# Performance work log

Hardware: AMD Instinct MI355X
Metric: run time of the kernel (lower is better)

The kernel has to match this reference:

```python
import jax, jax.numpy as jnp
import numpy as np

N = 100000   # nodes
E = 1600000  # edges
IN = 128     # in_dim
H = 64       # hidden_dim
EPS = 1e-5


def layer_norm(x, g, b):
    mu = x.mean(-1, keepdims=True)
    v = ((x - mu) ** 2).mean(-1, keepdims=True)
    return (x - mu) * jax.lax.rsqrt(v + EPS) * g + b


def gcn_conv(x, W, b, src, dst, dinv):
    # PyG GCNConv: x' = D^{-1/2}(A+I)D^{-1/2} X W + b (degrees include self-loops)
    h = x @ W                                   # [N, H]
    coef = dinv[src] * dinv[dst]                # [E]
    agg = jax.ops.segment_sum(h[src] * coef[:, None], dst, num_segments=N)
    agg = agg + h * (dinv * dinv)[:, None]      # self-loop term
    return agg + b


def setup_inputs() -> dict:
    key = jax.random.key(0)
    ks = jax.random.split(key, 12)
    inp = {
        "x": jax.random.normal(ks[0], (N, IN), jnp.float32),
        "edge_index": jax.random.randint(ks[1], (2, E), 0, N, dtype=jnp.int64
                                         if jax.config.jax_enable_x64 else jnp.int32),
    }
    dims = [(IN, H), (H, H), (H, H)]
    for i, (di, do) in enumerate(dims, start=1):
        inp[f"W{i}"] = jax.random.normal(ks[2 * i], (di, do), jnp.float32) / np.sqrt(di)
        inp[f"b{i}"] = jnp.zeros((do,), jnp.float32)
        inp[f"g{i}"] = jnp.ones((do,), jnp.float32)
        inp[f"be{i}"] = jnp.zeros((do,), jnp.float32)
    inp["Wh"] = jax.random.normal(ks[11], (H, 1), jnp.float32) / np.sqrt(H)
    inp["bh"] = jnp.zeros((1,), jnp.float32)
    return inp


def reference(x, edge_index, W1, b1, g1, be1, W2, b2, g2, be2, W3, b3, g3, be3, Wh, bh):
    src, dst = edge_index[0], edge_index[1]
    deg = jax.ops.segment_sum(jnp.ones((E,), x.dtype), dst, num_segments=N) + 1.0
    dinv = jax.lax.rsqrt(deg)
    for W, b, g, be in ((W1, b1, g1, be1), (W2, b2, g2, be2), (W3, b3, g3, be3)):
        x = gcn_conv(x, W, b, src, dst, dinv)
        x = layer_norm(x, g, be)
        x = jax.nn.gelu(x, approximate=False)  # F.gelu default = exact erf
        # dropout omitted (eval mode / deterministic reference)
    return (x @ Wh + bh).squeeze(-1)  # [N]
```

## Files before the change

### kernel.cpp

```cpp
#include <hip/hip_runtime.h>
#include <math.h>

#define NODES 100000
#define EDGES 1600000
#define SCAN_CHUNK 1024
#define NBUCK 196
#define BCAP2 12288
#define EPB 4096

typedef __attribute__((ext_vector_type(8))) short short8;
typedef __attribute__((ext_vector_type(4))) float floatx4;
typedef __attribute__((ext_vector_type(4))) unsigned uv4;

__device__ __forceinline__ float gsum8(float x) {
#pragma unroll
  for (int o = 4; o > 0; o >>= 1) x += __shfl_xor(x, o, 64);
  return x;
}

__device__ __forceinline__ short f2bf(float f) {
  union { float f; unsigned u; } v;
  v.f = f;
  unsigned r = 0x7fffu + ((v.u >> 16) & 1u);
  return (short)((v.u + r) >> 16);
}
__device__ __forceinline__ float bflo(unsigned p) {
  union { unsigned u; float f; } v; v.u = p << 16; return v.f;
}
__device__ __forceinline__ float bfhi(unsigned p) {
  union { unsigned u; float f; } v; v.u = p & 0xffff0000u; return v.f;
}

__global__ __launch_bounds__(256) void k_bin2(const int* __restrict__ src,
                                              const int* __restrict__ dst,
                                              int* __restrict__ bins,
                                              int* __restrict__ gcur) {
  __shared__ int cnt[NBUCK], gbase[NBUCK], lcur[NBUCK];
  int t = threadIdx.x;
  for (int i = t; i < NBUCK; i += 256) cnt[i] = 0;
  __syncthreads();
  int base = blockIdx.x * EPB;
  int s[16], d[16];
#pragma unroll
  for (int j = 0; j < 16; ++j) {
    int e = base + j * 256 + t;
    if (e < EDGES) {
      s[j] = src[e];
      d[j] = dst[e];
      atomicAdd(&cnt[d[j] >> 9], 1);
    } else {
      d[j] = -1;
    }
  }
  __syncthreads();
  for (int i = t; i < NBUCK; i += 256) {
    int c = cnt[i];
    gbase[i] = c ? atomicAdd(&gcur[i], c) : 0;
    lcur[i] = 0;
  }
  __syncthreads();
#pragma unroll
  for (int j = 0; j < 16; ++j) {
    if (d[j] >= 0) {
      int bk = d[j] >> 9;
      int lp = atomicAdd(&lcur[bk], 1);
      int pos = gbase[bk] + lp;
      if (pos < BCAP2) bins[bk * BCAP2 + pos] = s[j] | ((d[j] & 511) << 17);
    }
  }
}

__global__ __launch_bounds__(256) void k_hist(const int* __restrict__ bins,
                                              const int* __restrict__ gcur,
                                              int* __restrict__ deg,
                                              float* __restrict__ dinv) {
  __shared__ int cnt[512];
  int b = blockIdx.x, t = threadIdx.x;
  cnt[t] = 0; cnt[t + 256] = 0;
  __syncthreads();
  int c = gcur[b]; if (c > BCAP2) c = BCAP2;
  const int* bp = &bins[b * BCAP2];
  for (int i = t; i < c; i += 256)
    atomicAdd(&cnt[(bp[i] >> 17) & 511], 1);
  __syncthreads();
#pragma unroll
  for (int k = 0; k < 2; ++k) {
    int n = b * 512 + t + k * 256;
    if (n < NODES) {
      int cc = cnt[t + k * 256];
      deg[n] = cc;
      dinv[n] = rsqrtf((float)cc + 1.0f);
    }
  }
}

__global__ void k_scan1(const int* __restrict__ deg, int* __restrict__ part) {
  __shared__ int sw[4];
  int b = blockIdx.x, t = threadIdx.x;
  int base = b * SCAN_CHUNK;
  int s = 0;
#pragma unroll
  for (int j = 0; j < 4; ++j) {
    int i = base + t * 4 + j;
    if (i < NODES) s += deg[i];
  }
  for (int o = 32; o > 0; o >>= 1) s += __shfl_xor(s, o, 64);
  if ((t & 63) == 0) sw[t >> 6] = s;
  __syncthreads();
  if (t == 0) part[b] = sw[0] + sw[1] + sw[2] + sw[3];
}

__global__ void k_scan2(int* part, int nb) {
  __shared__ int sm[128];
  int t = threadIdx.x;
  int v = (t < nb) ? part[t] : 0;
  sm[t] = v;
  __syncthreads();
  for (int o = 1; o < 128; o <<= 1) {
    int u = (t >= o) ? sm[t - o] : 0;
    __syncthreads();
    sm[t] += u;
    __syncthreads();
  }
  if (t < nb) part[t] = sm[t] - v;
}

__global__ void k_scan3(const int* __restrict__ deg, const int* __restrict__ part,
                        int* __restrict__ rowptr) {
  __shared__ int wtot[4];
  int b = blockIdx.x, t = threadIdx.x;
  int lane = t & 63, wid = t >> 6;
  int base = b * SCAN_CHUNK;
  int d[4];
  int s = 0;
#pragma unroll
  for (int j = 0; j < 4; ++j) {
    int i = base + t * 4 + j;
    d[j] = (i < NODES) ? deg[i] : 0;
    s += d[j];
  }
  int inc = s;
#pragma unroll
  for (int o = 1; o < 64; o <<= 1) {
    int u = __shfl_up(inc, o, 64);
    if (lane >= o) inc += u;
  }
  if (lane == 63) wtot[wid] = inc;
  __syncthreads();
  int wpre = 0;
  for (int w = 0; w < wid; ++w) wpre += wtot[w];
  int off = part[b] + wpre + inc - s;
#pragma unroll
  for (int j = 0; j < 4; ++j) {
    int i = base + t * 4 + j;
    if (i < NODES) { rowptr[i] = off; off += d[j]; }
  }
  if (b == 0 && t == 0) rowptr[NODES] = EDGES;
}

__global__ __launch_bounds__(256) void k_fillb(const int* __restrict__ bins,
                                               const int* __restrict__ gcur,
                                               const int* __restrict__ rowptr,
                                               int* __restrict__ csr) {
  __shared__ int cur[512];
  int b = blockIdx.x, t = threadIdx.x;
#pragma unroll
  for (int k = 0; k < 2; ++k) {
    int n = b * 512 + t + k * 256;
    cur[t + k * 256] = (n < NODES) ? rowptr[n] : 0;
  }
  __syncthreads();
  int c = gcur[b]; if (c > BCAP2) c = BCAP2;
  const int* bp = &bins[b * BCAP2];
  for (int i = t; i < c; i += 256) {
    int pk = bp[i];
    int p = atomicAdd(&cur[(pk >> 17) & 511], 1);
    csr[p] = pk & 0x1FFFF;
  }
}

template <int K>
__global__ __launch_bounds__(256) void k_gemm_f32(const float* __restrict__ x,
                                                  const float* __restrict__ W,
                                                  const float* __restrict__ dinv,
                                                  short* __restrict__ hs) {
  constexpr int KP = K + 8;
  __shared__ short wt[64 * KP];
  for (int idx = threadIdx.x; idx < K * 64; idx += 256) {
    int k = idx >> 6, n = idx & 63;
    wt[n * KP + k] = f2bf(W[idx]);
  }
  __syncthreads();
  int wid = threadIdx.x >> 6, lane = threadIdx.x & 63;
  int tile = blockIdx.x * 4 + wid;
  if (tile * 16 >= NODES) return;
  int m = lane & 15, q = lane >> 4;

  short8 bfr[4][K / 32];
#pragma unroll
  for (int ct = 0; ct < 4; ++ct)
#pragma unroll
    for (int ks = 0; ks < K / 32; ++ks)
      bfr[ct][ks] = *reinterpret_cast<const short8*>(&wt[(ct * 16 + m) * KP + ks * 32 + q * 8]);

  floatx4 acc[4];
#pragma unroll
  for (int ct = 0; ct < 4; ++ct) acc[ct] = {0.f, 0.f, 0.f, 0.f};
  int r0 = tile * 16;
#pragma unroll
  for (int ks = 0; ks < K / 32; ++ks) {
    const float* xp = &x[(size_t)(r0 + m) * K + ks * 32 + q * 8];
    floatx4 a0 = *reinterpret_cast<const floatx4*>(xp);
    floatx4 a1 = *reinterpret_cast<const floatx4*>(xp + 4);
    short8 af;
#pragma unroll
    for (int j = 0; j < 4; ++j) { af[j] = f2bf(a0[j]); af[4 + j] = f2bf(a1[j]); }
#pragma unroll
    for (int ct = 0; ct < 4; ++ct)
      acc[ct] = __builtin_amdgcn_mfma_f32_16x16x32_bf16(af, bfr[ct][ks], acc[ct], 0, 0, 0);
  }
  float dv[4];
#pragma unroll
  for (int r = 0; r < 4; ++r) dv[r] = dinv[r0 + q * 4 + r];
#pragma unroll
  for (int ct = 0; ct < 4; ++ct)
#pragma unroll
    for (int r = 0; r < 4; ++r) {
      int row = r0 + q * 4 + r, col = ct * 16 + m;
      hs[row * 64 + col] = f2bf(acc[ct][r] * dv[r]);
    }
}

__global__ __launch_bounds__(256) void k_gemm_bf(const short* __restrict__ x,
                                                 const float* __restrict__ W,
                                                 const float* __restrict__ dinv,
                                                 short* __restrict__ hs) {
  constexpr int K = 64, KP = K + 8;
  __shared__ short wt[64 * KP];
  for (int idx = threadIdx.x; idx < K * 64; idx += 256) {
    int k = idx >> 6, n = idx & 63;
    wt[n * KP + k] = f2bf(W[idx]);
  }
  __syncthreads();
  int wid = threadIdx.x >> 6, lane = threadIdx.x & 63;
  int tile = blockIdx.x * 4 + wid;
  if (tile * 16 >= NODES) return;
  int m = lane & 15, q = lane >> 4;

  short8 bfr[4][2];
#pragma unroll
  for (int ct = 0; ct < 4; ++ct)
#pragma unroll
    for (int ks = 0; ks < 2; ++ks)
      bfr[ct][ks] = *reinterpret_cast<const short8*>(&wt[(ct * 16 + m) * KP + ks * 32 + q * 8]);

  floatx4 acc[4];
#pragma unroll
  for (int ct = 0; ct < 4; ++ct) acc[ct] = {0.f, 0.f, 0.f, 0.f};
  int r0 = tile * 16;
#pragma unroll
  for (int ks = 0; ks < 2; ++ks) {
    short8 af = *reinterpret_cast<const short8*>(&x[(size_t)(r0 + m) * K + ks * 32 + q * 8]);
#pragma unroll
    for (int ct = 0; ct < 4; ++ct)
      acc[ct] = __builtin_amdgcn_mfma_f32_16x16x32_bf16(af, bfr[ct][ks], acc[ct], 0, 0, 0);
  }
  float dv[4];
#pragma unroll
  for (int r = 0; r < 4; ++r) dv[r] = dinv[r0 + q * 4 + r];
#pragma unroll
  for (int ct = 0; ct < 4; ++ct)
#pragma unroll
    for (int r = 0; r < 4; ++r) {
      int row = r0 + q * 4 + r, col = ct * 16 + m;
      hs[row * 64 + col] = f2bf(acc[ct][r] * dv[r]);
    }
}

template <int FINAL>
__global__ __launch_bounds__(256) void k_agg(const short* __restrict__ hs,
                                             const float* __restrict__ dinv,
                                             const int* __restrict__ rowptr,
                                             const int* __restrict__ csr,
                                             const float* __restrict__ bias,
                                             const float* __restrict__ gam,
                                             const float* __restrict__ bet,
                                             const float* __restrict__ Wh,
                                             const float* __restrict__ bh,
                                             void* __restrict__ out) {
  const uv4* hsv = (const uv4*)hs;
  int lane = threadIdx.x & 63, wid = threadIdx.x >> 6;
  int g = lane >> 3, q = lane & 7;
  int n = blockIdx.x * 32 + wid * 8 + g;
  int e0 = rowptr[n], e1 = rowptr[n + 1];
  float dn = dinv[n];
  uv4 sv = hsv[(size_t)n * 8 + q];
  float acc[8];
#pragma unroll
  for (int w = 0; w < 4; ++w) { acc[2 * w] = bflo(sv[w]); acc[2 * w + 1] = bfhi(sv[w]); }

  int srcb = lane & 0x38;
  for (int base = e0; base < e1; base += 8) {
    int cnt = e1 - base;
    if (cnt > 8) cnt = 8;
    int a = base + (q < cnt ? q : 0);
    int sidx = csr[a];
    int s[8];
#pragma unroll
    for (int j = 0; j < 8; ++j) s[j] = __shfl(sidx, srcb | j, 64);
    uv4 v[8];
#pragma unroll
    for (int j = 0; j < 8; ++j) v[j] = hsv[(size_t)s[j] * 8 + q];
    if (cnt == 8) {
#pragma unroll
      for (int j = 0; j < 8; ++j)
#pragma unroll
        for (int w = 0; w < 4; ++w) { acc[2 * w] += bflo(v[j][w]); acc[2 * w + 1] += bfhi(v[j][w]); }
    } else {
#pragma unroll
      for (int j = 0; j < 8; ++j)
        if (j < cnt)
#pragma unroll
          for (int w = 0; w < 4; ++w) { acc[2 * w] += bflo(v[j][w]); acc[2 * w + 1] += bfhi(v[j][w]); }
    }
  }

  const floatx4* bi4 = (const floatx4*)bias;
  floatx4 b0 = bi4[q * 2], b1 = bi4[q * 2 + 1];
#pragma unroll
  for (int f = 0; f < 4; ++f) { acc[f] = acc[f] * dn + b0[f]; acc[f + 4] = acc[f + 4] * dn + b1[f]; }

  float lsum = 0.f;
#pragma unroll
  for (int f = 0; f < 8; ++f) lsum += acc[f];
  float mu = gsum8(lsum) * (1.0f / 64.0f);
  float d[8], lvar = 0.f;
#pragma unroll
  for (int f = 0; f < 8; ++f) { d[f] = acc[f] - mu; lvar += d[f] * d[f]; }
  float rs = rsqrtf(gsum8(lvar) * (1.0f / 64.0f) + 1e-5f);
  const floatx4* gm4 = (const floatx4*)gam;
  const floatx4* bt4 = (const floatx4*)bet;
  floatx4 g0 = gm4[q * 2], g1 = gm4[q * 2 + 1];
  floatx4 t0 = bt4[q * 2], t1 = bt4[q * 2 + 1];
  float u[8];
#pragma unroll
  for (int f = 0; f < 8; ++f) {
    float gv = (f < 4) ? g0[f] : g1[f - 4];
    float tv = (f < 4) ? t0[f] : t1[f - 4];
    float vv = d[f] * rs * gv + tv;
    u[f] = 0.5f * vv * (1.0f + erff(vv * 0.70710678118654752f));
  }
  if (FINAL) {
    const floatx4* wh4 = (const floatx4*)Wh;
    floatx4 w0 = wh4[q * 2], w1 = wh4[q * 2 + 1];
    float lp = 0.f;
#pragma unroll
    for (int f = 0; f < 4; ++f) lp += u[f] * w0[f] + u[f + 4] * w1[f];
    float p = gsum8(lp);
    if (q == 0) ((float*)out)[n] = p + bh[0];
  } else {
    uv4 pk;
#pragma unroll
    for (int w = 0; w < 4; ++w)
      pk[w] = (unsigned)(unsigned short)f2bf(u[2 * w]) |
              ((unsigned)(unsigned short)f2bf(u[2 * w + 1]) << 16);
    ((uv4*)out)[(size_t)n * 8 + q] = pk;
  }
}

extern "C" void kernel_launch(void* const* d_in, const int* in_sizes, int n_in,
                              void* d_out, int out_size, void* d_ws, size_t ws_size,
                              hipStream_t stream) {
  const float* x  = (const float*)d_in[0];
  const int* ei   = (const int*)d_in[1];
  const float* W1 = (const float*)d_in[2];
  const float* b1 = (const float*)d_in[3];
  const float* g1 = (const float*)d_in[4];
  const float* be1= (const float*)d_in[5];
  const float* W2 = (const float*)d_in[6];
  const float* b2 = (const float*)d_in[7];
  const float* g2 = (const float*)d_in[8];
  const float* be2= (const float*)d_in[9];
  const float* W3 = (const float*)d_in[10];
  const float* b3 = (const float*)d_in[11];
  const float* g3 = (const float*)d_in[12];
  const float* be3= (const float*)d_in[13];
  const float* Wh = (const float*)d_in[14];
  const float* bh = (const float*)d_in[15];
  const int* srcp = ei;
  const int* dstp = ei + EDGES;

  char* ws = (char*)d_ws;
  size_t off = 0;
  auto take = [&](size_t bytes) {
    char* p = ws + off;
    off = (off + bytes + 255) & ~(size_t)255;
    return p;
  };
  int* deg    = (int*)take((size_t)NODES * 4);
  float* dinv = (float*)take((size_t)NODES * 4);
  int* rowptr = (int*)take((size_t)(NODES + 1) * 4);
  int* part   = (int*)take(512);
  int* csr    = (int*)take((size_t)EDGES * 4);
  short* hs   = (short*)take((size_t)NODES * 64 * 2);
  short* xb   = (short*)take((size_t)NODES * 64 * 2);
  int* bins   = (int*)hs;
  int* gcur   = (int*)xb;

  (void)hipMemsetAsync(gcur, 0, (size_t)NBUCK * 4, stream);
  k_bin2<<<(EDGES + EPB - 1) / EPB, 256, 0, stream>>>(srcp, dstp, bins, gcur);
  k_hist<<<NBUCK, 256, 0, stream>>>(bins, gcur, deg, dinv);
  int nb = (NODES + SCAN_CHUNK - 1) / SCAN_CHUNK;
  k_scan1<<<nb, 256, 0, stream>>>(deg, part);
  k_scan2<<<1, 128, 0, stream>>>(part, nb);
  k_scan3<<<nb, 256, 0, stream>>>(deg, part, rowptr);
  k_fillb<<<NBUCK, 256, 0, stream>>>(bins, gcur, rowptr, csr);

  int gemm_grid = (NODES / 16 + 3) / 4;
  k_gemm_f32<128><<<gemm_grid, 256, 0, stream>>>(x, W1, dinv, hs);
  k_agg<0><<<NODES / 32, 256, 0, stream>>>(hs, dinv, rowptr, csr, b1, g1, be1, nullptr, nullptr, xb);
  k_gemm_bf<<<gemm_grid, 256, 0, stream>>>(xb, W2, dinv, hs);
  k_agg<0><<<NODES / 32, 256, 0, stream>>>(hs, dinv, rowptr, csr, b2, g2, be2, nullptr, nullptr, xb);
  k_gemm_bf<<<gemm_grid, 256, 0, stream>>>(xb, W3, dinv, hs);
  k_agg<1><<<NODES / 32, 256, 0, stream>>>(hs, dinv, rowptr, csr, b3, g3, be3, Wh, bh, d_out);
}
```

Before: 298.6 us.

## Fuse histogram, node scan and CSR fill via per-bucket base offsets

Replaces the histogram, three-pass node-degree scan and CSR fill kernels with a single-block scan over bucket counts plus one fused kernel per bucket. That kernel counts degrees in shared memory, scans them locally to produce rowptr and dinv, then scatters the edges into the CSR. Launch count drops from five kernels to two and the global deg array round trips go away. In exchange each bucket's bins are read twice inside one kernel, and the CSR build now depends on a serial single-block bucket scan.

```diff
diff --git a/kernel.cpp b/kernel.cpp
--- a/kernel.cpp
+++ b/kernel.cpp
@@ -3,7 +3,6 @@
 
 #define NODES 100000
 #define EDGES 1600000
-#define SCAN_CHUNK 1024
 #define NBUCK 196
 #define BCAP2 12288
 #define EPB 4096
@@ -70,108 +69,63 @@
   }
 }
 
-__global__ __launch_bounds__(256) void k_hist(const int* __restrict__ bins,
-                                              const int* __restrict__ gcur,
-                                              int* __restrict__ deg,
-                                              float* __restrict__ dinv) {
-  __shared__ int cnt[512];
-  int b = blockIdx.x, t = threadIdx.x;
-  cnt[t] = 0; cnt[t + 256] = 0;
-  __syncthreads();
-  int c = gcur[b]; if (c > BCAP2) c = BCAP2;
-  const int* bp = &bins[b * BCAP2];
-  for (int i = t; i < c; i += 256)
-    atomicAdd(&cnt[(bp[i] >> 17) & 511], 1);
-  __syncthreads();
-#pragma unroll
-  for (int k = 0; k < 2; ++k) {
-    int n = b * 512 + t + k * 256;
-    if (n < NODES) {
-      int cc = cnt[t + k * 256];
-      deg[n] = cc;
-      dinv[n] = rsqrtf((float)cc + 1.0f);
-    }
-  }
-}
-
-__global__ void k_scan1(const int* __restrict__ deg, int* __restrict__ part) {
-  __shared__ int sw[4];
-  int b = blockIdx.x, t = threadIdx.x;
-  int base = b * SCAN_CHUNK;
-  int s = 0;
-#pragma unroll
-  for (int j = 0; j < 4; ++j) {
-    int i = base + t * 4 + j;
-    if (i < NODES) s += deg[i];
-  }
-  for (int o = 32; o > 0; o >>= 1) s += __shfl_xor(s, o, 64);
-  if ((t & 63) == 0) sw[t >> 6] = s;
-  __syncthreads();
-  if (t == 0) part[b] = sw[0] + sw[1] + sw[2] + sw[3];
-}
-
-__global__ void k_scan2(int* part, int nb) {
-  __shared__ int sm[128];
+__global__ void k_scanb(const int* __restrict__ gcur, int* __restrict__ bbase,
+                        int* __restrict__ rowptr) {
+  __shared__ int sm[256];
   int t = threadIdx.x;
-  int v = (t < nb) ? part[t] : 0;
+  int v = 0;
+  if (t < NBUCK) { v = gcur[t]; if (v > BCAP2) v = BCAP2; }
   sm[t] = v;
   __syncthreads();
-  for (int o = 1; o < 128; o <<= 1) {
+  for (int o = 1; o < 256; o <<= 1) {
     int u = (t >= o) ? sm[t - o] : 0;
     __syncthreads();
     sm[t] += u;
     __syncthreads();
   }
-  if (t < nb) part[t] = sm[t] - v;
-}
-
-__global__ void k_scan3(const int* __restrict__ deg, const int* __restrict__ part,
-                        int* __restrict__ rowptr) {
-  __shared__ int wtot[4];
+  if (t < NBUCK) bbase[t] = sm[t] - v;
+  if (t == NBUCK - 1) {
+    bbase[NBUCK] = sm[t];
+    rowptr[NODES] = sm[t];
+  }
+}
+
+__global__ __launch_bounds__(256) void k_fillb2(const int* __restrict__ bins,
+                                                const int* __restrict__ gcur,
+                                                const int* __restrict__ bbase,
+                                                int* __restrict__ rowptr,
+                                                float* __restrict__ dinv,
+                                                int* __restrict__ csr) {
+  __shared__ int cnt[512], cur[512], wtot[4];
   int b = blockIdx.x, t = threadIdx.x;
-  int lane = t & 63, wid = t >> 6;
-  int base = b * SCAN_CHUNK;
-  int d[4];
-  int s = 0;
-#pragma unroll
-  for (int j = 0; j < 4; ++j) {
-    int i = base + t * 4 + j;
-    d[j] = (i < NODES) ? deg[i] : 0;
-    s += d[j];
-  }
+  cnt[t] = 0; cnt[t + 256] = 0;
+  __syncthreads();
+  int c = gcur[b]; if (c > BCAP2) c = BCAP2;
+  const int* bp = &bins[(size_t)b * BCAP2];
+  for (int i = t; i < c; i += 256)
+    atomicAdd(&cnt[(bp[i] >> 17) & 511], 1);
+  __syncthreads();
+  int a0 = cnt[2 * t], a1 = cnt[2 * t + 1];
+  int s = a0 + a1;
+  int lane = t & 63, w = t >> 6;
   int inc = s;
 #pragma unroll
   for (int o = 1; o < 64; o <<= 1) {
     int u = __shfl_up(inc, o, 64);
     if (lane >= o) inc += u;
   }
-  if (lane == 63) wtot[wid] = inc;
+  if (lane == 63) wtot[w] = inc;
   __syncthreads();
   int wpre = 0;
-  for (int w = 0; w < wid; ++w) wpre += wtot[w];
-  int off = part[b] + wpre + inc - s;
-#pragma unroll
-  for (int j = 0; j < 4; ++j) {
-    int i = base + t * 4 + j;
-    if (i < NODES) { rowptr[i] = off; off += d[j]; }
-  }
-  if (b == 0 && t == 0) rowptr[NODES] = EDGES;
-}
-
-__global__ __launch_bounds__(256) void k_fillb(const int* __restrict__ bins,
-                                               const int* __restrict__ gcur,
-                                               const int* __restrict__ rowptr,
-                                               int* __restrict__ csr) {
-  __shared__ int cur[512];
-  int b = blockIdx.x, t = threadIdx.x;
-#pragma unroll
-  for (int k = 0; k < 2; ++k) {
-    int n = b * 512 + t + k * 256;
-    cur[t + k * 256] = (n < NODES) ? rowptr[n] : 0;
-  }
-  __syncthreads();
-  int c = gcur[b]; if (c > BCAP2) c = BCAP2;
-  const int* bp = &bins[b * BCAP2];
+  for (int ww = 0; ww < w; ++ww) wpre += wtot[ww];
+  int base = bbase[b];
+  int r0 = base + wpre + inc - s;
+  int r1 = r0 + a0;
+  int n0 = b * 512 + 2 * t, n1 = n0 + 1;
+  if (n0 < NODES) { rowptr[n0] = r0; dinv[n0] = rsqrtf((float)a0 + 1.0f); }
+  if (n1 < NODES) { rowptr[n1] = r1; dinv[n1] = rsqrtf((float)a1 + 1.0f); }
+  cur[2 * t] = r0; cur[2 * t + 1] = r1;
+  __syncthreads();
   for (int i = t; i < c; i += 256) {
     int pk = bp[i];
     int p = atomicAdd(&cur[(pk >> 17) & 511], 1);
@@ -397,10 +351,9 @@
     off = (off + bytes + 255) & ~(size_t)255;
     return p;
   };
-  int* deg    = (int*)take((size_t)NODES * 4);
   float* dinv = (float*)take((size_t)NODES * 4);
   int* rowptr = (int*)take((size_t)(NODES + 1) * 4);
-  int* part   = (int*)take(512);
+  int* bbase  = (int*)take((size_t)(NBUCK + 1) * 4);
   int* csr    = (int*)take((size_t)EDGES * 4);
   short* hs   = (short*)take((size_t)NODES * 64 * 2);
   short* xb   = (short*)take((size_t)NODES * 64 * 2);
@@ -409,12 +362,8 @@
 
   (void)hipMemsetAsync(gcur, 0, (size_t)NBUCK * 4, stream);
   k_bin2<<<(EDGES + EPB - 1) / EPB, 256, 0, stream>>>(srcp, dstp, bins, gcur);
-  k_hist<<<NBUCK, 256, 0, stream>>>(bins, gcur, deg, dinv);
-  int nb = (NODES + SCAN_CHUNK - 1) / SCAN_CHUNK;
-  k_scan1<<<nb, 256, 0, stream>>>(deg, part);
-  k_scan2<<<1, 128, 0, stream>>>(part, nb);
-  k_scan3<<<nb, 256, 0, stream>>>(deg, part, rowptr);
-  k_fillb<<<NBUCK, 256, 0, stream>>>(bins, gcur, rowptr, csr);
+  k_scanb<<<1, 256, 0, stream>>>(gcur, bbase, rowptr);
+  k_fillb2<<<NBUCK, 256, 0, stream>>>(bins, gcur, bbase, rowptr, dinv, csr);
 
   int gemm_grid = (NODES / 16 + 3) / 4;
   k_gemm_f32<128><<<gemm_grid, 256, 0, stream>>>(x, W1, dinv, hs);
```

Result: no change. 292.8 us (-1.9%).
